# Kernel optimization log

Hardware: AMD Instinct MI355X
Metric: run time of the kernel (lower is better)

The kernel has to match this reference:

```python
import jax, jax.numpy as jnp
import numpy as np

N = 100000          # nodes
E = 1600000         # edges
DIMS = [128, 64, 64, 47]  # in_feats -> hidden -> hidden -> n_classes
EPS = 1e-5


def setup_inputs() -> dict:
    key = jax.random.key(0)
    ks = jax.random.split(key, 10)
    d = {
        "features": jax.random.normal(ks[0], (N, DIMS[0]), jnp.float32),
        "src": jax.random.randint(ks[1], (E,), 0, N, dtype=jnp.int64),
        "dst": jax.random.randint(ks[2], (E,), 0, N, dtype=jnp.int64),
    }
    # GraphConv weights (glorot-ish) + bias
    for i in range(3):
        fan_in, fan_out = DIMS[i], DIMS[i + 1]
        scale = jnp.sqrt(2.0 / (fan_in + fan_out)).astype(jnp.float32)
        d[f"W{i}"] = jax.random.normal(ks[3 + i], (fan_in, fan_out), jnp.float32) * scale
        d[f"b{i}"] = jnp.zeros((fan_out,), jnp.float32)
    # BatchNorm affine params for the first two layers
    for i in range(2):
        d[f"gamma{i}"] = jnp.ones((DIMS[i + 1],), jnp.float32)
        d[f"beta{i}"] = jnp.zeros((DIMS[i + 1],), jnp.float32)
    return d


def _degree_isqrt(idx):
    # clamp degree to >=1 like DGL, then D^{-1/2}
    deg = jax.ops.segment_sum(jnp.ones((E,), jnp.float32), idx, num_segments=N)
    return jax.lax.rsqrt(jnp.maximum(deg, 1.0))


def _graph_conv(h, W, b, src, dst, out_isqrt, in_isqrt):
    # DGL GraphConv, norm='both': h' = D_in^{-1/2} A D_out^{-1/2} h W + b
    h = h * out_isqrt[:, None]
    if W.shape[0] > W.shape[1]:  # mult W first when it shrinks features (DGL order)
        h = h @ W
        h = jax.ops.segment_sum(h[src], dst, num_segments=N)
    else:
        h = jax.ops.segment_sum(h[src], dst, num_segments=N)
        h = h @ W
    return h * in_isqrt[:, None] + b


def _batch_norm(h, gamma, beta):
    mu = h.mean(axis=0)
    var = h.var(axis=0)  # biased, as torch BatchNorm uses for normalization
    return gamma * (h - mu) * jax.lax.rsqrt(var + EPS) + beta


def reference(features, src, dst, W0, b0, W1, b1, W2, b2,
              gamma0, beta0, gamma1, beta1):
    out_isqrt = _degree_isqrt(src)
    in_isqrt = _degree_isqrt(dst)
    Ws = [(W0, b0), (W1, b1), (W2, b2)]
    bns = [(gamma0, beta0), (gamma1, beta1)]
    h = features
    for i, (W, b) in enumerate(Ws):
        # dropout (p=0.5) before last layer only -> identity in eval mode
        h = _graph_conv(h, W, b, src, dst, out_isqrt, in_isqrt)
        if i < len(Ws) - 1:
            h = _batch_norm(h, *bns[i])
            h = jax.nn.relu(h)
    return h
```

## Files before the change

### kernel.cpp

```cpp
#include <hip/hip_runtime.h>
#include <hip/hip_bf16.h>
#include <hip/hip_fp16.h>

#define BN_EPS 1e-5f
#define N_MAX 100000
#define CAP 64
#define NB_MAX 391
#define BCAP 8192

typedef __attribute__((ext_vector_type(8))) _Float16 half8;
typedef __attribute__((ext_vector_type(4))) float floatx4;

__device__ float g_wsf[130 * N_MAX + 256];
__device__ int   g_wsi[(1 + CAP) * N_MAX + NB_MAX * BCAP + 2 * NB_MAX + 64];
__device__ unsigned char g_wsb[NB_MAX * BCAP];

__global__ __launch_bounds__(256)
void k_bin(const int* __restrict__ src, const int* __restrict__ dst,
           int* __restrict__ gcur, int* __restrict__ scur,
           int* __restrict__ pairs, unsigned char* __restrict__ sbytes,
           int E, int nb) {
    __shared__ int dh[NB_MAX], db[NB_MAX], dc[NB_MAX];
    __shared__ int sh[NB_MAX], sb[NB_MAX], sc[NB_MAX];
    const int tid = threadIdx.x;
    for (int i = tid; i < nb; i += 256) { dh[i] = 0; sh[i] = 0; dc[i] = 0; sc[i] = 0; }
    __syncthreads();
    const int e0 = blockIdx.x * 4096;
    int ss[16], dd[16];
#pragma unroll
    for (int i = 0; i < 16; ++i) {
        int e = e0 + i * 256 + tid;
        if (e < E) {
            ss[i] = src[e]; dd[i] = dst[e];
            atomicAdd(&dh[dd[i] >> 8], 1);
            atomicAdd(&sh[ss[i] >> 8], 1);
        } else ss[i] = -1;
    }
    __syncthreads();
    for (int i = tid; i < nb; i += 256) {
        db[i] = atomicAdd(&gcur[i], dh[i]);
        sb[i] = atomicAdd(&scur[i], sh[i]);
    }
    __syncthreads();
#pragma unroll
    for (int i = 0; i < 16; ++i) {
        if (ss[i] >= 0) {
            int b = dd[i] >> 8;
            int idx = db[b] + atomicAdd(&dc[b], 1);
            if (idx < BCAP) pairs[b * BCAP + idx] = (ss[i] << 8) | (dd[i] & 255);
            int b2 = ss[i] >> 8;
            int i2 = sb[b2] + atomicAdd(&sc[b2], 1);
            if (i2 < BCAP) sbytes[b2 * BCAP + i2] = (unsigned char)(ss[i] & 255);
        }
    }
}

__global__ __launch_bounds__(256)
void k_slab(const int* __restrict__ gcur, const int* __restrict__ pairs,
            int* __restrict__ slab, int* __restrict__ cnt,
            float* __restrict__ isq_d, int n) {
    __shared__ int c[256];
    const int tid = threadIdx.x;
    const int d0 = blockIdx.x * 256;
    c[tid] = 0;
    __syncthreads();
    const int m = min(gcur[blockIdx.x], BCAP);
    const int base = blockIdx.x * BCAP;
    for (int i = tid; i < m; i += 256) {
        int p = pairs[base + i];
        int dl = p & 255;
        int slot = atomicAdd(&c[dl], 1);
        if (slot < CAP) slab[(size_t)(d0 + dl) * CAP + slot] = p >> 8;
    }
    __syncthreads();
    int d = d0 + tid;
    if (d < n) {
        cnt[d] = c[tid];
        isq_d[d] = rsqrtf(fmaxf((float)c[tid], 1.0f));
    }
}

__global__ __launch_bounds__(256)
void k_degs(const int* __restrict__ scur, const unsigned char* __restrict__ sbytes,
            float* __restrict__ isq_s, int n) {
    __shared__ int c[256];
    const int tid = threadIdx.x;
    c[tid] = 0;
    __syncthreads();
    const int m = min(scur[blockIdx.x], BCAP);
    const int base = blockIdx.x * BCAP;
    for (int i = tid; i < m; i += 256) atomicAdd(&c[sbytes[base + i]], 1);
    __syncthreads();
    int s = blockIdx.x * 256 + tid;
    if (s < n) isq_s[s] = rsqrtf(fmaxf((float)c[tid], 1.0f));
}

template<bool SB>
__global__ __launch_bounds__(256)
void k_agg(const int* __restrict__ cnt, const int* __restrict__ slab,
           const __half* __restrict__ in, const float* __restrict__ isq_d,
           const float* __restrict__ bias, __half* __restrict__ out, int n) {
    const int d = (int)((blockIdx.x * 256u + threadIdx.x) >> 6);
    if (d >= n) return;
    const int lane = threadIdx.x & 63;
    const int sub = lane >> 3;
    const int fc = (lane & 7) << 3;
    const int m = min(cnt[d], CAP);
    const int* cs = slab + (size_t)d * CAP;
    float a0 = 0.0f, a1 = 0.0f, a2 = 0.0f, a3 = 0.0f;
    float a4 = 0.0f, a5 = 0.0f, a6 = 0.0f, a7 = 0.0f;
    for (int e = 0; e < m; e += 16) {
#pragma unroll
        for (int u = 0; u < 2; ++u) {
            int j = e + u * 8 + sub;
            if (j < m) {
                int s = cs[j];
                const uint4 v = *(const uint4*)(in + (size_t)s * 64 + fc);
                const float2 f0 = __half22float2(*(const __half2*)&v.x);
                const float2 f1 = __half22float2(*(const __half2*)&v.y);
                const float2 f2 = __half22float2(*(const __half2*)&v.z);
                const float2 f3 = __half22float2(*(const __half2*)&v.w);
                a0 += f0.x; a1 += f0.y; a2 += f1.x; a3 += f1.y;
                a4 += f2.x; a5 += f2.y; a6 += f3.x; a7 += f3.y;
            }
        }
    }
#pragma unroll
    for (int sh = 8; sh <= 32; sh <<= 1) {
        a0 += __shfl_xor(a0, sh); a1 += __shfl_xor(a1, sh);
        a2 += __shfl_xor(a2, sh); a3 += __shfl_xor(a3, sh);
        a4 += __shfl_xor(a4, sh); a5 += __shfl_xor(a5, sh);
        a6 += __shfl_xor(a6, sh); a7 += __shfl_xor(a7, sh);
    }
    if (sub == 0) {
        if (SB) {
            const float sd = isq_d[d];
            const float4 b0 = *(const float4*)(bias + fc);
            const float4 b1 = *(const float4*)(bias + fc + 4);
            a0 = a0 * sd + b0.x; a1 = a1 * sd + b0.y;
            a2 = a2 * sd + b0.z; a3 = a3 * sd + b0.w;
            a4 = a4 * sd + b1.x; a5 = a5 * sd + b1.y;
            a6 = a6 * sd + b1.z; a7 = a7 * sd + b1.w;
        }
        __half2 h01 = __floats2half2_rn(a0, a1);
        __half2 h23 = __floats2half2_rn(a2, a3);
        __half2 h45 = __floats2half2_rn(a4, a5);
        __half2 h67 = __floats2half2_rn(a6, a7);
        uint4 u;
        u.x = *(const unsigned*)&h01; u.y = *(const unsigned*)&h23;
        u.z = *(const unsigned*)&h45; u.w = *(const unsigned*)&h67;
        *(uint4*)(out + (size_t)d * 64 + fc) = u;
    }
}

template<int KIN, int KOUTR, bool HIN, bool HOUT, bool BIAS>
__global__ __launch_bounds__(256)
void k_gemm_mfma(const void* __restrict__ Xv, const float* __restrict__ rowscale,
                 const float* __restrict__ W, const float* __restrict__ bias,
                 void* __restrict__ Cv, int n) {
    constexpr int NK = KIN / 32;
    constexpr int NT = (KOUTR + 15) / 16;
    constexpr int CHUNKS = KIN / 8;
    __shared__ __align__(16) unsigned short Xs[64 * KIN];
    const int tid = threadIdx.x;
    const int row0 = blockIdx.x * 64;

#pragma unroll
    for (int it = 0; it < (64 * CHUNKS) / 256; ++it) {
        const int idx = it * 256 + tid;
        const int row = idx / CHUNKS;
        const int ch = idx & (CHUNKS - 1);
        const int rg = row0 + row;
        uint4 v = {0u, 0u, 0u, 0u};
        if (rg < n) {
            if (HIN) {
                v = *(const uint4*)((const __half*)Xv + (size_t)rg * KIN + ch * 8);
            } else {
                const float* Xf = (const float*)Xv;
                const float4 f0 = *(const float4*)(Xf + (size_t)rg * KIN + ch * 8);
                const float4 f1 = *(const float4*)(Xf + (size_t)rg * KIN + ch * 8 + 4);
                __half2 h01 = __floats2half2_rn(f0.x, f0.y);
                __half2 h23 = __floats2half2_rn(f0.z, f0.w);
                __half2 h45 = __floats2half2_rn(f1.x, f1.y);
                __half2 h67 = __floats2half2_rn(f1.z, f1.w);
                v.x = *(const unsigned*)&h01; v.y = *(const unsigned*)&h23;
                v.z = *(const unsigned*)&h45; v.w = *(const unsigned*)&h67;
            }
        }
        const int sch = ch ^ (row & 7);
        *(uint4*)(&Xs[row * KIN + sch * 8]) = v;
    }

    const int lane = tid & 63;
    const int lc = lane & 15;
    const int lg = lane >> 4;
    half8 bf[NK][NT];
#pragma unroll
    for (int s = 0; s < NK; ++s)
#pragma unroll
        for (int t = 0; t < NT; ++t)
#pragma unroll
            for (int j = 0; j < 8; ++j) {
                const int k = s * 32 + lg * 8 + j;
                const int c = t * 16 + lc;
                const float wv = (c < KOUTR) ? W[k * KOUTR + c] : 0.0f;
                bf[s][t][j] = (_Float16)wv;
            }

    __syncthreads();

    const int w = tid >> 6;
    const int rowl = 16 * w + lc;
    floatx4 acc[NT];
#pragma unroll
    for (int t = 0; t < NT; ++t) acc[t] = 0.0f;
#pragma unroll
    for (int s = 0; s < NK; ++s) {
        const int ch = s * 4 + lg;
        const int sch = ch ^ (rowl & 7);
        const half8 a = *(const half8*)(&Xs[rowl * KIN + sch * 8]);
#pragma unroll
        for (int t = 0; t < NT; ++t)
            acc[t] = __builtin_amdgcn_mfma_f32_16x16x32_f16(a, bf[s][t], acc[t], 0, 0, 0);
    }

    const int rbase = row0 + 16 * w + lg * 4;
#pragma unroll
    for (int t = 0; t < NT; ++t) {
        const int c = t * 16 + lc;
#pragma unroll
        for (int r = 0; r < 4; ++r) {
            const int rg = rbase + r;
            if (rg >= n) continue;
            float v = acc[t][r] * rowscale[rg];
            if (BIAS) v += bias[c];
            if (HOUT) {
                ((__half*)Cv)[(size_t)rg * KOUTR + c] = __float2half_rn(v);
            } else {
                if (KOUTR == 64 || c < KOUTR)
                    ((float*)Cv)[(size_t)rg * KOUTR + c] = v;
            }
        }
    }
}

template<bool HIN>
__global__ __launch_bounds__(256)
void k_bn_stats(const void* __restrict__ Av, float* __restrict__ stats, int n) {
    const int f = threadIdx.x & 63;
    const int sub = threadIdx.x >> 6;
    float s = 0.0f, q = 0.0f;
    for (int i = blockIdx.x * 4 + sub; i < n; i += gridDim.x * 4) {
        float h;
        if (HIN) h = __half2float(((const __half*)Av)[(size_t)i * 64 + f]);
        else     h = ((const float*)Av)[(size_t)i * 64 + f];
        s += h;
        q += h * h;
    }
    __shared__ float ls[4][64], lq[4][64];
    ls[sub][f] = s; lq[sub][f] = q;
    __syncthreads();
    if (sub == 0) {
        s = ls[0][f] + ls[1][f] + ls[2][f] + ls[3][f];
        q = lq[0][f] + lq[1][f] + lq[2][f] + lq[3][f];
        atomicAdd(&stats[f], s);
        atomicAdd(&stats[64 + f], q);
    }
}

template<bool HIN>
__global__ __launch_bounds__(256)
void k_bn_apply(const void* __restrict__ Av, const float* __restrict__ gamma,
                const float* __restrict__ beta, const float* __restrict__ stats,
                const float* __restrict__ outscale, __half* __restrict__ B, int n) {
    unsigned gid = blockIdx.x * 256u + threadIdx.x;
    unsigned i = gid >> 4;
    if (i >= (unsigned)n) return;
    unsigned fq = (gid & 15u) << 2;
    const float invn = 1.0f / (float)n;
    const float4 sm = *(const float4*)(stats + fq);
    const float4 sq = *(const float4*)(stats + 64 + fq);
    const float4 g  = *(const float4*)(gamma + fq);
    const float4 be = *(const float4*)(beta + fq);
    float4 h;
    if (HIN) {
        const uint2 u = *(const uint2*)((const __half*)Av + (size_t)i * 64 + fq);
        const float2 p0 = __half22float2(*(const __half2*)&u.x);
        const float2 p1 = __half22float2(*(const __half2*)&u.y);
        h.x = p0.x; h.y = p0.y; h.z = p1.x; h.w = p1.y;
    } else {
        h = *(const float4*)((const float*)Av + (size_t)i * 64 + fq);
    }
    const float os = outscale[i];
    float4 r;
    { float mu = sm.x * invn, var = sq.x * invn - mu * mu;
      r.x = fmaxf(g.x * (h.x - mu) * rsqrtf(var + BN_EPS) + be.x, 0.0f) * os; }
    { float mu = sm.y * invn, var = sq.y * invn - mu * mu;
      r.y = fmaxf(g.y * (h.y - mu) * rsqrtf(var + BN_EPS) + be.y, 0.0f) * os; }
    { float mu = sm.z * invn, var = sq.z * invn - mu * mu;
      r.z = fmaxf(g.z * (h.z - mu) * rsqrtf(var + BN_EPS) + be.z, 0.0f) * os; }
    { float mu = sm.w * invn, var = sq.w * invn - mu * mu;
      r.w = fmaxf(g.w * (h.w - mu) * rsqrtf(var + BN_EPS) + be.w, 0.0f) * os; }
    __half2 h01 = __floats2half2_rn(r.x, r.y);
    __half2 h23 = __floats2half2_rn(r.z, r.w);
    uint2 u;
    u.x = *(const unsigned*)&h01;
    u.y = *(const unsigned*)&h23;
    *(uint2*)(B + (size_t)i * 64 + fq) = u;
}

extern "C" void kernel_launch(void* const* d_in, const int* in_sizes, int n_in,
                              void* d_out, int out_size, void* d_ws, size_t ws_size,
                              hipStream_t stream) {
    const float* feat = (const float*)d_in[0];
    const int* src  = (const int*)d_in[1];
    const int* dst  = (const int*)d_in[2];
    const float* W0  = (const float*)d_in[3];
    const float* b0  = (const float*)d_in[4];
    const float* W1  = (const float*)d_in[5];
    const float* b1  = (const float*)d_in[6];
    const float* W2  = (const float*)d_in[7];
    const float* b2  = (const float*)d_in[8];
    const float* g0  = (const float*)d_in[9];
    const float* be0 = (const float*)d_in[10];
    const float* g1  = (const float*)d_in[11];
    const float* be1 = (const float*)d_in[12];

    const int n = out_size / 47;
    const int E = in_sizes[1];
    const int nb = (n + 255) >> 8;

    float* wsf = nullptr; int* wsi = nullptr; unsigned char* wsb = nullptr;
    hipGetSymbolAddress((void**)&wsf, HIP_SYMBOL(g_wsf));
    hipGetSymbolAddress((void**)&wsi, HIP_SYMBOL(g_wsi));
    hipGetSymbolAddress((void**)&wsb, HIP_SYMBOL(g_wsb));
    float* isq_s = wsf;
    float* isq_d = wsf + n;
    float* buf1  = wsf + 2 * (size_t)n;
    float* buf2  = buf1 + (size_t)n * 64;
    float* stats = buf2 + (size_t)n * 64;
    __half* buf1h = (__half*)buf1;
    __half* buf2h = (__half*)buf2;
    int* cnt     = wsi;
    int* slab    = wsi + n;
    int* pairs   = wsi + (size_t)(1 + CAP) * n;
    int* gcur    = pairs + (size_t)NB_MAX * BCAP;
    int* scur    = gcur + NB_MAX;

    const int gB = (E + 4095) / 4096;
    const int gW = (n + 3) / 4;
    const int gG = (n + 63) / 64;
    const int gA = (n * 16 + 255) / 256;

    hipMemsetAsync(gcur, 0, 2 * NB_MAX * sizeof(int), stream);
    hipMemsetAsync(stats, 0, 256 * sizeof(float), stream);
    k_bin<<<gB, 256, 0, stream>>>(src, dst, gcur, scur, pairs, wsb, E, nb);
    k_slab<<<nb, 256, 0, stream>>>(gcur, pairs, slab, cnt, isq_d, n);
    k_degs<<<nb, 256, 0, stream>>>(scur, wsb, isq_s, n);

    k_gemm_mfma<128, 64, false, true, false><<<gG, 256, 0, stream>>>(feat, isq_s, W0, nullptr, buf1h, n);
    k_agg<true><<<gW, 256, 0, stream>>>(cnt, slab, buf1h, isq_d, b0, buf2h, n);
    k_bn_stats<true><<<512, 256, 0, stream>>>(buf2h, stats, n);
    k_bn_apply<true><<<gA, 256, 0, stream>>>(buf2h, g0, be0, stats, isq_s, buf1h, n);

    k_agg<false><<<gW, 256, 0, stream>>>(cnt, slab, buf1h, nullptr, nullptr, buf2h, n);
    k_gemm_mfma<64, 64, true, false, true><<<gG, 256, 0, stream>>>(buf2h, isq_d, W1, b1, buf1, n);
    k_bn_stats<false><<<512, 256, 0, stream>>>(buf1, stats + 128, n);
    k_bn_apply<false><<<gA, 256, 0, stream>>>(buf1, g1, be1, stats + 128, isq_s, buf2h, n);

    k_agg<false><<<gW, 256, 0, stream>>>(cnt, slab, buf2h, nullptr, nullptr, buf1h, n);
    k_gemm_mfma<64, 47, true, false, true><<<gG, 256, 0, stream>>>(buf1h, isq_d, W2, b2, (float*)d_out, n);
}
```

Measured before the change: 468.2 us.

## Replace binned CSR build with direct global-atomic slab fill; pretranspose weights

Swaps the three-kernel binning pipeline (local histogram, pair buffer, per-bin slab fill, separate source-degree pass) for a single grid-stride kernel that does a global atomicAdd per edge on the destination count and source degree and writes the source straight into the destination's slab. It also adds a small kernel that transposes and converts the weights to fp16 once, so each GEMM block loads its B fragments with vector reads instead of strided scalar float loads. This removes the intermediate pair and byte buffers and one pass over the edges. In exchange it takes heavily contended random global atomics and scattered slab writes, and slab order becomes nondeterministic.

```diff
diff --git a/kernel.cpp b/kernel.cpp
--- a/kernel.cpp
+++ b/kernel.cpp
@@ -5,94 +5,52 @@
 #define BN_EPS 1e-5f
 #define N_MAX 100000
 #define CAP 64
-#define NB_MAX 391
-#define BCAP 8192
 
 typedef __attribute__((ext_vector_type(8))) _Float16 half8;
 typedef __attribute__((ext_vector_type(4))) float floatx4;
 
-__device__ float g_wsf[130 * N_MAX + 256];
-__device__ int   g_wsi[(1 + CAP) * N_MAX + NB_MAX * BCAP + 2 * NB_MAX + 64];
-__device__ unsigned char g_wsb[NB_MAX * BCAP];
-
-__global__ __launch_bounds__(256)
-void k_bin(const int* __restrict__ src, const int* __restrict__ dst,
-           int* __restrict__ gcur, int* __restrict__ scur,
-           int* __restrict__ pairs, unsigned char* __restrict__ sbytes,
-           int E, int nb) {
-    __shared__ int dh[NB_MAX], db[NB_MAX], dc[NB_MAX];
-    __shared__ int sh[NB_MAX], sb[NB_MAX], sc[NB_MAX];
-    const int tid = threadIdx.x;
-    for (int i = tid; i < nb; i += 256) { dh[i] = 0; sh[i] = 0; dc[i] = 0; sc[i] = 0; }
-    __syncthreads();
-    const int e0 = blockIdx.x * 4096;
-    int ss[16], dd[16];
-#pragma unroll
-    for (int i = 0; i < 16; ++i) {
-        int e = e0 + i * 256 + tid;
-        if (e < E) {
-            ss[i] = src[e]; dd[i] = dst[e];
-            atomicAdd(&dh[dd[i] >> 8], 1);
-            atomicAdd(&sh[ss[i] >> 8], 1);
-        } else ss[i] = -1;
-    }
-    __syncthreads();
-    for (int i = tid; i < nb; i += 256) {
-        db[i] = atomicAdd(&gcur[i], dh[i]);
-        sb[i] = atomicAdd(&scur[i], sh[i]);
-    }
-    __syncthreads();
-#pragma unroll
-    for (int i = 0; i < 16; ++i) {
-        if (ss[i] >= 0) {
-            int b = dd[i] >> 8;
-            int idx = db[b] + atomicAdd(&dc[b], 1);
-            if (idx < BCAP) pairs[b * BCAP + idx] = (ss[i] << 8) | (dd[i] & 255);
-            int b2 = ss[i] >> 8;
-            int i2 = sb[b2] + atomicAdd(&sc[b2], 1);
-            if (i2 < BCAP) sbytes[b2 * BCAP + i2] = (unsigned char)(ss[i] & 255);
-        }
-    }
-}
-
-__global__ __launch_bounds__(256)
-void k_slab(const int* __restrict__ gcur, const int* __restrict__ pairs,
-            int* __restrict__ slab, int* __restrict__ cnt,
-            float* __restrict__ isq_d, int n) {
-    __shared__ int c[256];
-    const int tid = threadIdx.x;
-    const int d0 = blockIdx.x * 256;
-    c[tid] = 0;
-    __syncthreads();
-    const int m = min(gcur[blockIdx.x], BCAP);
-    const int base = blockIdx.x * BCAP;
-    for (int i = tid; i < m; i += 256) {
-        int p = pairs[base + i];
-        int dl = p & 255;
-        int slot = atomicAdd(&c[dl], 1);
-        if (slot < CAP) slab[(size_t)(d0 + dl) * CAP + slot] = p >> 8;
-    }
-    __syncthreads();
-    int d = d0 + tid;
-    if (d < n) {
-        cnt[d] = c[tid];
-        isq_d[d] = rsqrtf(fmaxf((float)c[tid], 1.0f));
-    }
-}
-
-__global__ __launch_bounds__(256)
-void k_degs(const int* __restrict__ scur, const unsigned char* __restrict__ sbytes,
-            float* __restrict__ isq_s, int n) {
-    __shared__ int c[256];
-    const int tid = threadIdx.x;
-    c[tid] = 0;
-    __syncthreads();
-    const int m = min(scur[blockIdx.x], BCAP);
-    const int base = blockIdx.x * BCAP;
-    for (int i = tid; i < m; i += 256) atomicAdd(&c[sbytes[base + i]], 1);
-    __syncthreads();
-    int s = blockIdx.x * 256 + tid;
-    if (s < n) isq_s[s] = rsqrtf(fmaxf((float)c[tid], 1.0f));
+__device__ __attribute__((aligned(16))) float g_wsf[130 * N_MAX + 16384];
+__device__ int   g_wsi[(2 + CAP) * N_MAX + 64];
+
+__global__ __launch_bounds__(256)
+void k_build(const int* __restrict__ src, const int* __restrict__ dst,
+             int* __restrict__ cnt, int* __restrict__ degs,
+             int* __restrict__ slab, int E) {
+    int e = blockIdx.x * 256 + threadIdx.x;
+    const int stride = gridDim.x * 256;
+    for (; e < E; e += stride) {
+        const int s = src[e];
+        const int d = dst[e];
+        atomicAdd(&degs[s], 1);
+        const int slot = atomicAdd(&cnt[d], 1);
+        if (slot < CAP) slab[(size_t)d * CAP + slot] = s;
+    }
+}
+
+__global__ __launch_bounds__(256)
+void k_isq(const int* __restrict__ cnt, const int* __restrict__ degs,
+           float* __restrict__ isq_d, float* __restrict__ isq_s, int n) {
+    const int i = blockIdx.x * 256 + threadIdx.x;
+    if (i < n) {
+        isq_d[i] = rsqrtf(fmaxf((float)cnt[i], 1.0f));
+        isq_s[i] = rsqrtf(fmaxf((float)degs[i], 1.0f));
+    }
+}
+
+__device__ void wt_fill(const float* __restrict__ W, __half* __restrict__ Wt,
+                        int KIN, int KOUT, int ROWS) {
+    for (int i = threadIdx.x; i < ROWS * KIN; i += 256) {
+        const int c = i / KIN, k = i - c * KIN;
+        Wt[c * KIN + k] = (c < KOUT) ? __float2half_rn(W[k * KOUT + c]) : __float2half_rn(0.0f);
+    }
+}
+__global__ __launch_bounds__(256)
+void k_wprep(const float* __restrict__ W0, const float* __restrict__ W1,
+             const float* __restrict__ W2, __half* __restrict__ Wt0,
+             __half* __restrict__ Wt1, __half* __restrict__ Wt2) {
+    if (blockIdx.x == 0)      wt_fill(W0, Wt0, 128, 64, 64);
+    else if (blockIdx.x == 1) wt_fill(W1, Wt1, 64, 64, 64);
+    else                      wt_fill(W2, Wt2, 64, 47, 48);
 }
 
 template<bool SB>
@@ -156,7 +114,7 @@
 template<int KIN, int KOUTR, bool HIN, bool HOUT, bool BIAS>
 __global__ __launch_bounds__(256)
 void k_gemm_mfma(const void* __restrict__ Xv, const float* __restrict__ rowscale,
-                 const float* __restrict__ W, const float* __restrict__ bias,
+                 const __half* __restrict__ Wt, const float* __restrict__ bias,
                  void* __restrict__ Cv, int n) {
     constexpr int NK = KIN / 32;
     constexpr int NT = (KOUTR + 15) / 16;
@@ -199,13 +157,7 @@
     for (int s = 0; s < NK; ++s)
 #pragma unroll
         for (int t = 0; t < NT; ++t)
-#pragma unroll
-            for (int j = 0; j < 8; ++j) {
-                const int k = s * 32 + lg * 8 + j;
-                const int c = t * 16 + lc;
-                const float wv = (c < KOUTR) ? W[k * KOUTR + c] : 0.0f;
-                bf[s][t][j] = (_Float16)wv;
-            }
+            bf[s][t] = *(const half8*)(Wt + (size_t)(t * 16 + lc) * KIN + s * 32 + lg * 8);
 
     __syncthreads();
 
@@ -328,46 +280,45 @@
 
     const int n = out_size / 47;
     const int E = in_sizes[1];
-    const int nb = (n + 255) >> 8;
-
-    float* wsf = nullptr; int* wsi = nullptr; unsigned char* wsb = nullptr;
+
+    float* wsf = nullptr; int* wsi = nullptr;
     hipGetSymbolAddress((void**)&wsf, HIP_SYMBOL(g_wsf));
     hipGetSymbolAddress((void**)&wsi, HIP_SYMBOL(g_wsi));
-    hipGetSymbolAddress((void**)&wsb, HIP_SYMBOL(g_wsb));
     float* isq_s = wsf;
     float* isq_d = wsf + n;
     float* buf1  = wsf + 2 * (size_t)n;
     float* buf2  = buf1 + (size_t)n * 64;
     float* stats = buf2 + (size_t)n * 64;
+    __half* Wt0  = (__half*)(stats + 256);
+    __half* Wt1  = Wt0 + 64 * 128;
+    __half* Wt2  = Wt1 + 64 * 64;
     __half* buf1h = (__half*)buf1;
     __half* buf2h = (__half*)buf2;
     int* cnt     = wsi;
-    int* slab    = wsi + n;
-    int* pairs   = wsi + (size_t)(1 + CAP) * n;
-    int* gcur    = pairs + (size_t)NB_MAX * BCAP;
-    int* scur    = gcur + NB_MAX;
-
-    const int gB = (E + 4095) / 4096;
+    int* degs    = wsi + n;
+    int* slab    = wsi + 2 * (size_t)n;
+
     const int gW = (n + 3) / 4;
     const int gG = (n + 63) / 64;
     const int gA = (n * 16 + 255) / 256;
-
-    hipMemsetAsync(gcur, 0, 2 * NB_MAX * sizeof(int), stream);
+    const int gN = (n + 255) / 256;
+
+    hipMemsetAsync(cnt, 0, 2 * (size_t)n * sizeof(int), stream);
     hipMemsetAsync(stats, 0, 256 * sizeof(float), stream);
-    k_bin<<<gB, 256, 0, stream>>>(src, dst, gcur, scur, pairs, wsb, E, nb);
-    k_slab<<<nb, 256, 0, stream>>>(gcur, pairs, slab, cnt, isq_d, n);
-    k_degs<<<nb, 256, 0, stream>>>(scur, wsb, isq_s, n);
-
-    k_gemm_mfma<128, 64, false, true, false><<<gG, 256, 0, stream>>>(feat, isq_s, W0, nullptr, buf1h, n);
+    k_wprep<<<3, 256, 0, stream>>>(W0, W1, W2, Wt0, Wt1, Wt2);
+    k_build<<<1024, 256, 0, stream>>>(src, dst, cnt, degs, slab, E);
+    k_isq<<<gN, 256, 0, stream>>>(cnt, degs, isq_d, isq_s, n);
+
+    k_gemm_mfma<128, 64, false, true, false><<<gG, 256, 0, stream>>>(feat, isq_s, Wt0, nullptr, buf1h, n);
     k_agg<true><<<gW, 256, 0, stream>>>(cnt, slab, buf1h, isq_d, b0, buf2h, n);
     k_bn_stats<true><<<512, 256, 0, stream>>>(buf2h, stats, n);
     k_bn_apply<true><<<gA, 256, 0, stream>>>(buf2h, g0, be0, stats, isq_s, buf1h, n);
 
     k_agg<false><<<gW, 256, 0, stream>>>(cnt, slab, buf1h, nullptr, nullptr, buf2h, n);
-    k_gemm_mfma<64, 64, true, false, true><<<gG, 256, 0, stream>>>(buf2h, isq_d, W1, b1, buf1, n);
+    k_gemm_mfma<64, 64, true, false, true><<<gG, 256, 0, stream>>>(buf2h, isq_d, Wt1, b1, buf1, n);
     k_bn_stats<false><<<512, 256, 0, stream>>>(buf1, stats + 128, n);
     k_bn_apply<false><<<gA, 256, 0, stream>>>(buf1, g1, be1, stats + 128, isq_s, buf2h, n);
 
     k_agg<false><<<gW, 256, 0, stream>>>(cnt, slab, buf2h, nullptr, nullptr, buf1h, n);
-    k_gemm_mfma<64, 47, true, false, true><<<gG, 256, 0, stream>>>(buf1h, isq_d, W2, b2, (float*)d_out, n);
-}
+    k_gemm_mfma<64, 47, true, false, true><<<gG, 256, 0, stream>>>(buf1h, isq_d, Wt2, b2, (float*)d_out, n);
+}
```

Measured after the change: 553.4 us. 18.2% more time.
